# Kernel tuning notes

Hardware: AMD Instinct MI355X
Metric: run time of the kernel (lower is better)

## Reference

```python
import jax, jax.numpy as jnp
import numpy as np

LOG2PI = float(np.log(2.0 * np.pi))

def _sym(M):
    return (M + M.T) * 0.5

def setup_inputs() -> dict:
    key = jax.random.key(0)
    k = jax.random.split(key, 5)
    ntrials, v_dim, T, z_dim = 32, 64, 8192, 16
    v = jax.random.normal(k[0], (ntrials, v_dim, T), jnp.float32)
    # A scaled by 0.2 (instead of raw rand) so the 8192-step recursion stays numerically sane
    A = 0.2 * jax.random.uniform(k[1], (z_dim, z_dim), dtype=jnp.float32)
    B = 0.1 * jnp.eye(z_dim, dtype=jnp.float32)            # as in torch __init__
    W = jax.random.uniform(k[2], (v_dim, z_dim), dtype=jnp.float32)
    mu0 = jax.random.uniform(k[3], (z_dim,), dtype=jnp.float32)
    Sigma0_half = 0.1 * jnp.eye(z_dim, dtype=jnp.float32)  # as in torch __init__
    log_sigma_v = jnp.log(jnp.array([0.5], dtype=jnp.float32))
    return {"v": v, "A": A, "B": B, "W": W, "mu0": mu0,
            "Sigma0_half": Sigma0_half, "log_sigma_v": log_sigma_v}

def reference(v, A, B, W, mu0, Sigma0_half, log_sigma_v):
    # Forward pass used in Preprocessor.fit: kalman_covariance (smoothing=False)
    # + kalman_means (smoothing=False) + LL.  Returns LL per trial [ntrials].
    ntrials, v_dim, T = v.shape
    z_dim = A.shape[0]
    Iz = jnp.eye(z_dim, dtype=v.dtype)
    Iv = jnp.eye(v_dim, dtype=v.dtype)

    var_v = jnp.exp(log_sigma_v[0]) ** 2
    R = var_v * Iv + 1e-6 * Iv                       # property R
    Btri = jnp.tril(B)
    Q = Btri @ Btri.T + 1e-6 * Iz                    # property Q
    S0h = jnp.tril(Sigma0_half)
    Sigma0 = S0h @ S0h.T + 1e-6 * Iz                 # property Sigma0

    def rcho(Lc, X):  # X @ inv(Lc Lc.T), Lc lower cholesky (== chol_inv(..., left=False))
        return jax.scipy.linalg.cho_solve((Lc, True), X.T).T

    # ---- Kalman covariance recursion (data-independent) ----
    L0 = jnp.linalg.cholesky(R + W @ Sigma0 @ W.T)
    K0 = rcho(L0, Sigma0 @ W.T)                      # [z, v]
    Sf0 = _sym(Sigma0 - K0 @ W @ Sigma0)

    def cov_step(Sf, _):
        Sd = _sym(A @ Sf @ A.T + Q)                  # Sigma diffused
        L = jnp.linalg.cholesky(R + W @ Sd @ W.T + 1e-6 * Iv)
        K = rcho(L, Sd @ W.T)
        return _sym(Sd - K @ W @ Sd), (Sd, K)

    _, (Sigmas_diffused, Ks) = jax.lax.scan(cov_step, Sf0, None, length=T - 1)
    # Sigmas_diffused: [T-1, z, z], Ks: [T-1, z, v]

    # ---- Kalman means recursion (vectorized over trials) ----
    vT = jnp.moveaxis(v, -1, 0)                      # [T, ntrials, v_dim]
    muf0 = mu0 + (vT[0] - W @ mu0) @ K0.T            # [ntrials, z]

    def mean_step(muf, inp):
        K, x = inp
        mud = muf @ A.T
        return mud + (x - mud @ W.T) @ K.T, mud

    _, mus_diffused = jax.lax.scan(mean_step, muf0, (Ks, vT[1:]))  # [T-1, n, z]

    # ---- Log likelihood ----
    Lc0 = jnp.linalg.cholesky(W @ Sigma0 @ W.T + R)
    d0 = vT[0] - W @ mu0                             # [n, v]
    s0 = jax.scipy.linalg.solve_triangular(Lc0, d0.T, lower=True)  # [v, n]
    first = (-0.5 * v_dim * LOG2PI
             - jnp.sum(jnp.log(jnp.diag(Lc0)))
             - 0.5 * jnp.sum(s0 ** 2, axis=0))       # [n]

    ms = mus_diffused @ W.T                          # [T-1, n, v]
    covs = jnp.einsum('ij,tjk,lk->til', W, Sigmas_diffused, W) + R + 1e-6 * Iv
    Lt = jnp.linalg.cholesky(covs)                   # [T-1, v, v]
    diff = vT[1:] - ms                               # [T-1, n, v]
    sol = jax.vmap(lambda Lm, dm: jax.scipy.linalg.solve_triangular(Lm, dm.T, lower=True).T)(Lt, diff)
    logdet = jnp.sum(jnp.log(jnp.diagonal(Lt, axis1=-2, axis2=-1)), axis=-1)  # [T-1]
    second = (-0.5 * v_dim * LOG2PI - logdet[:, None]
              - 0.5 * jnp.sum(sol ** 2, axis=-1))    # [T-1, n]
    return first + jnp.sum(second, axis=0)           # [n]
```

## Files before the change

kernel.cpp:

```cpp
#include <hip/hip_runtime.h>
#include <math.h>


#define T_TOT 8192
#define NTR   32
#define VD    64
#define NCHUNK 512
#define CHLEN  16
#define NI     12

#define OFF_FS    8
#define OFF_S     16
#define OFF_P0    272
#define OFF_PSS   528
#define OFF_F     784
#define OFF_M16   1040
#define OFF_KQ    1296
#define OFF_EN0   1552
#define OFF_FQ    2064
#define OFF_VC    2096
#define OFF_QS    (OFF_VC + NCHUNK*512)
#define OFF_Q     (OFF_QS + NCHUNK*32)
#define OFF_XX    (OFF_Q + T_TOT*512)
#define WS_FLOATS (OFF_XX + T_TOT*32 + 64)

__device__ float g_wf[WS_FLOATS];

#define SWZ(x, imm) __int_as_float(__builtin_amdgcn_ds_swizzle(__float_as_int(x), (imm)))

#define MV16(row, vv, out) do { \
  float b0_=SWZ(vv,0x010), b1_=SWZ(vv,0x030), b2_=SWZ(vv,0x050), b3_=SWZ(vv,0x070); \
  float b4_=SWZ(vv,0x090), b5_=SWZ(vv,0x0B0), b6_=SWZ(vv,0x0D0), b7_=SWZ(vv,0x0F0); \
  float b8_=SWZ(vv,0x110), b9_=SWZ(vv,0x130), b10_=SWZ(vv,0x150), b11_=SWZ(vv,0x170); \
  float b12_=SWZ(vv,0x190), b13_=SWZ(vv,0x1B0), b14_=SWZ(vv,0x1D0), b15_=SWZ(vv,0x1F0); \
  float s0_=fmaf((row)[0],b0_,fmaf((row)[1],b1_,fmaf((row)[2],b2_,(row)[3]*b3_))); \
  float s1_=fmaf((row)[4],b4_,fmaf((row)[5],b5_,fmaf((row)[6],b6_,(row)[7]*b7_))); \
  float s2_=fmaf((row)[8],b8_,fmaf((row)[9],b9_,fmaf((row)[10],b10_,(row)[11]*b11_))); \
  float s3_=fmaf((row)[12],b12_,fmaf((row)[13],b13_,fmaf((row)[14],b14_,(row)[15]*b15_))); \
  (out)=(s0_+s1_)+(s2_+s3_); \
} while(0)

#define RED16(x) do { x+=SWZ(x,0x041F); x+=SWZ(x,0x081F); x+=SWZ(x,0x101F); x+=SWZ(x,0x201F); } while(0)

__device__ __forceinline__ void mm_reg(float* C, const float* Aa, const float* Bb, int lane)
{
  const int rowbase = lane & 0x3C;
  const int g = lane & 3;
  #pragma unroll
  for (int j = 0; j < 4; ++j) C[j] = 0.f;
  #pragma unroll
  for (int k = 0; k < 16; ++k) {
    float a = __shfl(Aa[k & 3], rowbase | (k >> 2), 64);
    #pragma unroll
    for (int j = 0; j < 4; ++j) {
      float b = __shfl(Bb[j], 4*k + g, 64);
      C[j] = fmaf(a, b, C[j]);
    }
  }
}

__device__ __forceinline__ void mmbt_reg(float* C, const float* Aa, const float* Bb, int lane)
{
  const int rowbase = lane & 0x3C;
  const int g = lane & 3;
  #pragma unroll
  for (int j = 0; j < 4; ++j) C[j] = 0.f;
  #pragma unroll
  for (int k = 0; k < 16; ++k) {
    float a = __shfl(Aa[k & 3], rowbase | (k >> 2), 64);
    #pragma unroll
    for (int j = 0; j < 4; ++j) {
      float bt = __shfl(Bb[k & 3], 16*g + 4*j + (k >> 2), 64);
      C[j] = fmaf(a, bt, C[j]);
    }
  }
}

__device__ __forceinline__ float gj_reg(float* M, float* R, int lane)
{
  const int i = lane >> 2;
  const int rowbase = lane & 0x3C;
  const int g = lane & 3;
  float ld = 0.f;
  #pragma unroll
  for (int k = 0; k < 16; ++k) {
    float p = __shfl(M[k & 3], 4*k + (k >> 2), 64);
    ld += __logf(fabsf(p));
    float r = 1.f / p;
    float f = __shfl(M[k & 3], rowbase | (k >> 2), 64) * r;
    float t = (i != k) ? f : 0.f;
    #pragma unroll
    for (int j = 0; j < 4; ++j) {
      float mk = __shfl(M[j], 4*k + g, 64);
      float rk = __shfl(R[j], 4*k + g, 64);
      M[j] = fmaf(-t, mk, M[j]);
      R[j] = fmaf(-t, rk, R[j]);
    }
  }
  int e = i & 3;
  float dm = (e & 2) ? ((e & 1) ? M[3] : M[2]) : ((e & 1) ? M[1] : M[0]);
  float d = __shfl(dm, 4*i + (i >> 2), 64);
  float rd = 1.f / d;
  #pragma unroll
  for (int j = 0; j < 4; ++j) R[j] *= rd;
  return ld;
}

__global__ __launch_bounds__(256) void k_front(const float* __restrict__ v,
                                               const float* __restrict__ A,
                                               const float* __restrict__ B,
                                               const float* __restrict__ W,
                                               const float* __restrict__ S0h,
                                               const float* __restrict__ lsv)
{
  const int tid = threadIdx.x;
  float* __restrict__ wf = g_wf;

  if (blockIdx.x != 0) {
    __shared__ float Wl[VD][16];
    for (int e = tid; e < VD*16; e += 256) Wl[e>>4][e&15] = W[e];
    __syncthreads();
    const int bid = blockIdx.x - 1;
    const int n = bid >> 4;
    const int t0 = (bid & 15)*512 + tid*2;
    const float* vp = v + (size_t)n*VD*T_TOT + t0;
    float a0[16], a1[16];
    #pragma unroll
    for (int k = 0; k < 16; ++k) { a0[k] = 0.f; a1[k] = 0.f; }
    float s20 = 0.f, s21 = 0.f;
    #pragma unroll 4
    for (int i2 = 0; i2 < VD; ++i2) {
      float2 x = *(const float2*)&vp[(size_t)i2*T_TOT];
      s20 = fmaf(x.x, x.x, s20); s21 = fmaf(x.y, x.y, s21);
      const float4* wr = (const float4*)&Wl[i2][0];
      float4 w0 = wr[0], w1 = wr[1], w2 = wr[2], w3 = wr[3];
      a0[0]=fmaf(x.x,w0.x,a0[0]);  a1[0]=fmaf(x.y,w0.x,a1[0]);
      a0[1]=fmaf(x.x,w0.y,a0[1]);  a1[1]=fmaf(x.y,w0.y,a1[1]);
      a0[2]=fmaf(x.x,w0.z,a0[2]);  a1[2]=fmaf(x.y,w0.z,a1[2]);
      a0[3]=fmaf(x.x,w0.w,a0[3]);  a1[3]=fmaf(x.y,w0.w,a1[3]);
      a0[4]=fmaf(x.x,w1.x,a0[4]);  a1[4]=fmaf(x.y,w1.x,a1[4]);
      a0[5]=fmaf(x.x,w1.y,a0[5]);  a1[5]=fmaf(x.y,w1.y,a1[5]);
      a0[6]=fmaf(x.x,w1.z,a0[6]);  a1[6]=fmaf(x.y,w1.z,a1[6]);
      a0[7]=fmaf(x.x,w1.w,a0[7]);  a1[7]=fmaf(x.y,w1.w,a1[7]);
      a0[8]=fmaf(x.x,w2.x,a0[8]);  a1[8]=fmaf(x.y,w2.x,a1[8]);
      a0[9]=fmaf(x.x,w2.y,a0[9]);  a1[9]=fmaf(x.y,w2.y,a1[9]);
      a0[10]=fmaf(x.x,w2.z,a0[10]); a1[10]=fmaf(x.y,w2.z,a1[10]);
      a0[11]=fmaf(x.x,w2.w,a0[11]); a1[11]=fmaf(x.y,w2.w,a1[11]);
      a0[12]=fmaf(x.x,w3.x,a0[12]); a1[12]=fmaf(x.y,w3.x,a1[12]);
      a0[13]=fmaf(x.x,w3.y,a0[13]); a1[13]=fmaf(x.y,w3.y,a1[13]);
      a0[14]=fmaf(x.x,w3.z,a0[14]); a1[14]=fmaf(x.y,w3.z,a1[14]);
      a0[15]=fmaf(x.x,w3.w,a0[15]); a1[15]=fmaf(x.y,w3.w,a1[15]);
    }
    float4* q0 = (float4*)(wf + OFF_Q + (size_t)n*131072 + (size_t)t0*16);
    q0[0] = make_float4(a0[0],a0[1],a0[2],a0[3]);
    q0[1] = make_float4(a0[4],a0[5],a0[6],a0[7]);
    q0[2] = make_float4(a0[8],a0[9],a0[10],a0[11]);
    q0[3] = make_float4(a0[12],a0[13],a0[14],a0[15]);
    q0[4] = make_float4(a1[0],a1[1],a1[2],a1[3]);
    q0[5] = make_float4(a1[4],a1[5],a1[6],a1[7]);
    q0[6] = make_float4(a1[8],a1[9],a1[10],a1[11]);
    q0[7] = make_float4(a1[12],a1[13],a1[14],a1[15]);
    wf[OFF_XX + (size_t)n*T_TOT + t0]     = s20;
    wf[OFF_XX + (size_t)n*T_TOT + t0 + 1] = s21;
    return;
  }

  __shared__ float Wl[VD][16];
  __shared__ float Al[16][16], Sm_l[16][16], Qm_l[16][16], S0_l[16][16];
  const int ri = tid >> 4, ci = tid & 15;
  for (int e = tid; e < VD*16; e += 256) Wl[e>>4][e&15] = W[e];
  Al[ri][ci] = A[tid];
  __syncthreads();
  {
    float s = 0.f;
    for (int r = 0; r < VD; ++r) s = fmaf(Wl[r][ri], Wl[r][ci], s);
    Sm_l[ri][ci] = s;
    int m = ri < ci ? ri : ci;
    float q = (ri==ci)?1e-6f:0.f, g0 = (ri==ci)?1e-6f:0.f;
    for (int r = 0; r <= m; ++r) {
      q  = fmaf(B[ri*16+r],   B[ci*16+r],   q);
      g0 = fmaf(S0h[ri*16+r], S0h[ci*16+r], g0);
    }
    Qm_l[ri][ci] = q;
    S0_l[ri][ci] = g0;
  }
  __syncthreads();
  if (tid >= 64) return;

  const int lane = tid;
  const int i = lane >> 2, g = lane & 3;
  float al[4], sm[4], qm[4], s0[4], scl[4], scl0[4], dmask[4];
  {
    float4 t;
    t = *(const float4*)&Al[i][4*g];   al[0]=t.x; al[1]=t.y; al[2]=t.z; al[3]=t.w;
    t = *(const float4*)&Sm_l[i][4*g]; sm[0]=t.x; sm[1]=t.y; sm[2]=t.z; sm[3]=t.w;
    t = *(const float4*)&Qm_l[i][4*g]; qm[0]=t.x; qm[1]=t.y; qm[2]=t.z; qm[3]=t.w;
    t = *(const float4*)&S0_l[i][4*g]; s0[0]=t.x; s0[1]=t.y; s0[2]=t.z; s0[3]=t.w;
  }
  #pragma unroll
  for (int j = 0; j < 4; ++j) dmask[j] = (4*g + j == i) ? 1.f : 0.f;

  float ev = expf(lsv[0]); float var = ev*ev;
  float c0v = var + 1e-6f, cv = var + 2e-6f;
  float invc0 = 1.f/c0v, invc = 1.f/cv;
  float logc = __logf(cv);
  #pragma unroll
  for (int j = 0; j < 4; ++j) { scl0[j] = sm[j]*invc0; scl[j] = sm[j]*invc; }

  float gm[4];
  mm_reg(gm, s0, scl0, lane);
  #pragma unroll
  for (int j = 0; j < 4; ++j) gm[j] += dmask[j];
  float ld0 = gj_reg(gm, s0, lane);
  float ldet_first = 0.5f*(64.f*__logf(c0v) + ld0);
  {
    float4* w4;
    w4 = (float4*)(wf + OFF_P0 + i*16 + 4*g); *w4 = make_float4(s0[0],s0[1],s0[2],s0[3]);
    w4 = (float4*)(wf + OFF_S  + i*16 + 4*g); *w4 = make_float4(sm[0],sm[1],sm[2],sm[3]);
  }

  float p[4];
  #pragma unroll
  for (int j = 0; j < 4; ++j) p[j] = s0[j];

  double dacc = 0.0; float ld_t = 0.f;
  float t1[4], sd[4];
  #pragma unroll 1
  for (int t = 0; t < NI; ++t) {
    mm_reg(t1, al, p, lane);
    mmbt_reg(sd, t1, al, lane);
    #pragma unroll
    for (int j = 0; j < 4; ++j) sd[j] += qm[j];
    mm_reg(gm, sd, scl, lane);
    #pragma unroll
    for (int j = 0; j < 4; ++j) gm[j] += dmask[j];
    float ldG = gj_reg(gm, sd, lane);
    #pragma unroll
    for (int j = 0; j < 4; ++j) p[j] = sd[j];
    ld_t = 0.5f*(64.f*logc + ldG);
    dacc += (double)ld_t;
  }
  double ldet_total = dacc + (double)(T_TOT-1-NI)*(double)ld_t;

  float kq[4], fm_[4], tB[4];
  mm_reg(t1, al, p, lane);
  #pragma unroll
  for (int j = 0; j < 4; ++j) kq[j] = t1[j]*invc;
  mm_reg(tB, kq, sm, lane);
  #pragma unroll
  for (int j = 0; j < 4; ++j) fm_[j] = al[j] - tB[j];
  {
    float4* w4;
    w4 = (float4*)(wf + OFF_PSS + i*16 + 4*g); *w4 = make_float4(p[0],p[1],p[2],p[3]);
    w4 = (float4*)(wf + OFF_F   + i*16 + 4*g); *w4 = make_float4(fm_[0],fm_[1],fm_[2],fm_[3]);
    w4 = (float4*)(wf + OFF_KQ  + i*16 + 4*g); *w4 = make_float4(kq[0],kq[1],kq[2],kq[3]);
  }
  mm_reg(t1, fm_, fm_, lane);
  mm_reg(tB, t1, t1, lane);
  mm_reg(t1, tB, tB, lane);
  mm_reg(tB, t1, t1, lane);
  {
    float4* w4 = (float4*)(wf + OFF_M16 + i*16 + 4*g);
    *w4 = make_float4(tB[0],tB[1],tB[2],tB[3]);
  }
  if (lane == 0) {
    double* d = (double*)wf;
    d[0] = (double)ldet_first;
    d[1] = ldet_total;
    wf[OFF_FS+0] = c0v; wf[OFF_FS+1] = cv; wf[OFF_FS+2] = invc; wf[OFF_FS+3] = invc0;
  }
}

__global__ __launch_bounds__(256) void k_passA(const float* __restrict__ A,
                                               const float* __restrict__ mu0)
{
  const int tid = threadIdx.x; const int j = tid & 15;
  const int n = blockIdx.y*16 + (tid >> 4);
  float* __restrict__ wf = g_wf;

  if (blockIdx.x == NCHUNK) {
    float Ar[16], Sr[16], P0r[16];
    #pragma unroll
    for (int k = 0; k < 16; ++k) {
      Ar[k]  = A[j*16+k];
      Sr[k]  = wf[OFF_S  + j*16 + k];
      P0r[k] = wf[OFF_P0 + j*16 + k];
    }
    const float invc0 = wf[OFF_FS+3];
    float mu0j = mu0[j];
    float q0  = wf[OFF_Q + (size_t)n*131072 + j];
    float xx0 = wf[OFF_XX + (size_t)n*T_TOT];
    float h0; MV16(Sr, mu0j, h0);
    float u0 = q0 - h0;
    float w0; MV16(P0r, u0, w0);
    float loc = fmaf(-2.f*q0, mu0j, fmaf(mu0j, h0, -(u0*w0*invc0)));
    RED16(loc);
    if (j == 0) wf[OFF_FQ + n] = (xx0 + loc)*invc0;
    float muf = fmaf(w0, invc0, mu0j);
    float en; MV16(Ar, muf, en);
    wf[OFF_EN0 + n*16 + j] = en;
    return;
  }

  const int chunk = blockIdx.x;
  float Fr[16], Kr[16];
  #pragma unroll
  for (int k = 0; k < 16; ++k) {
    Fr[k] = wf[OFF_F  + j*16 + k];
    Kr[k] = wf[OFF_KQ + j*16 + k];
  }
  const int t0 = 1 + CHLEN*chunk;
  const float* qp = wf + OFF_Q + (size_t)n*131072 + (size_t)t0*16 + j;
  float mud = 0.f;
  #pragma unroll
  for (int s = 0; s < CHLEN; ++s) {
    float qj = qp[s*16];
    float g; MV16(Kr, qj, g);
    float fm; MV16(Fr, mud, fm);
    mud = fm + g;
  }
  wf[OFF_VC + chunk*512 + n*16 + j] = mud;
}

__global__ __launch_bounds__(256) void k_passC(const float* __restrict__ A)
{
  const int tid = threadIdx.x; const int j = tid & 15;
  const int n = blockIdx.y*16 + (tid >> 4);
  const int chunk = blockIdx.x;
  float* __restrict__ wf = g_wf;
  float Ar[16], Sr[16], Pr[16], Mr[16];
  #pragma unroll
  for (int k = 0; k < 16; ++k) {
    Ar[k] = A[j*16+k];
    Sr[k] = wf[OFF_S   + j*16 + k];
    Pr[k] = wf[OFF_PSS + j*16 + k];
    Mr[k] = wf[OFF_M16 + j*16 + k];
  }
  const float invc = wf[OFF_FS+2];

  float mud;
  if (chunk == 0) {
    mud = wf[OFF_EN0 + n*16 + j];
  } else {
    float v1 = wf[OFF_VC + (chunk-1)*512 + n*16 + j];
    float x2 = (chunk == 1) ? wf[OFF_EN0 + n*16 + j]
                            : wf[OFF_VC + (chunk-2)*512 + n*16 + j];
    float x3 = (chunk == 2) ? wf[OFF_EN0 + n*16 + j]
             : (chunk >= 3) ? wf[OFF_VC + (chunk-3)*512 + n*16 + j] : 0.f;
    float m3; MV16(Mr, x3, m3);
    float y = x2 + m3;
    float m2; MV16(Mr, y, m2);
    mud = v1 + m2;
  }

  const int t0 = 1 + CHLEN*chunk;
  const int ns = (CHLEN < (T_TOT-1) - t0 + 1) ? CHLEN : ((T_TOT-1) - t0 + 1);
  const float* qp  = wf + OFF_Q  + (size_t)n*131072 + (size_t)t0*16 + j;
  const float* xxp = wf + OFF_XX + (size_t)n*T_TOT + t0;
  float qacc = 0.f;
  #pragma unroll 4
  for (int s = 0; s < CHLEN; ++s) {
    float qj = qp[s*16];
    float xxv = xxp[s];
    float h; MV16(Sr, mud, h);
    float u = qj - h;
    float w; MV16(Pr, u, w);
    float loc = fmaf(-2.f*qj, mud, fmaf(mud, h, -(u*w*invc)));
    RED16(loc);
    if (s < ns) qacc = fmaf(xxv + loc, invc, qacc);
    float tmp = fmaf(w, invc, mud);
    MV16(Ar, tmp, mud);
  }
  if (j == 0) wf[OFF_QS + chunk*32 + n] = qacc;
}

__global__ __launch_bounds__(256) void k_final(float* __restrict__ out)
{
  const int tid = threadIdx.x;
  const int slice = tid >> 5, n = tid & 31;
  const float* wf = g_wf;
  __shared__ double red[8][32];
  double acc = 0.0;
  #pragma unroll 8
  for (int k = 0; k < NCHUNK/8; ++k)
    acc += (double)wf[OFF_QS + (slice*(NCHUNK/8) + k)*32 + n];
  red[slice][n] = acc;
  __syncthreads();
  if (tid < 32) {
    const double* dsc = (const double*)wf;
    double a = (double)wf[OFF_FQ + tid];
    #pragma unroll
    for (int s = 0; s < 8; ++s) a += red[s][tid];
    const double LOG2PI = 1.8378770664093453;
    double ll = -32.0*LOG2PI*(double)T_TOT - dsc[0] - dsc[1] - 0.5*a;
    out[tid] = (float)ll;
  }
}

extern "C" void kernel_launch(void* const* d_in, const int* in_sizes, int n_in,
                              void* d_out, int out_size, void* d_ws, size_t ws_size,
                              hipStream_t stream)
{
  (void)in_sizes; (void)n_in; (void)out_size; (void)d_ws; (void)ws_size;
  const float* v   = (const float*)d_in[0];
  const float* A   = (const float*)d_in[1];
  const float* B   = (const float*)d_in[2];
  const float* W   = (const float*)d_in[3];
  const float* mu0 = (const float*)d_in[4];
  const float* S0h = (const float*)d_in[5];
  const float* lsv = (const float*)d_in[6];
  float* out = (float*)d_out;

  k_front<<<1 + NTR*16, 256, 0, stream>>>(v, A, B, W, S0h, lsv);
  k_passA<<<dim3(NCHUNK+1,2), 256, 0, stream>>>(A, mu0);
  k_passC<<<dim3(NCHUNK,2), 256, 0, stream>>>(A);
  k_final<<<1, 256, 0, stream>>>(out);
}
```

Measured before the change: 182.7 us.

## Use DPP/bpermute matrix ops, fewer warmup iterations, and F/K mean update in passC

Replaces the shuffle-based 16x16 register matrix multiply and Gauss-Jordan helpers with DPP quad broadcasts, ds_bpermute and readlane, and accumulates the determinant as a double product instead of summing per-pivot logs. Cuts the covariance warm-up iterations before steady state is assumed from 12 to 8. In passC, the mean update changes from A·(mud + w·invc) to F·mud + K·q, which matches passA. The Mr load also moves into the chunk>0 branch and the chunk loop is fully unrolled. Together these shorten the serial front kernel and the passC inner loop, but fewer warm-up steps risks a less accurate steady-state covariance.

```diff
diff --git a/kernel.cpp b/kernel.cpp
--- a/kernel.cpp
+++ b/kernel.cpp
@@ -7,7 +7,7 @@
 #define VD    64
 #define NCHUNK 512
 #define CHLEN  16
-#define NI     12
+#define NI     8
 
 #define OFF_FS    8
 #define OFF_S     16
@@ -42,68 +42,57 @@
 
 #define RED16(x) do { x+=SWZ(x,0x041F); x+=SWZ(x,0x081F); x+=SWZ(x,0x101F); x+=SWZ(x,0x201F); } while(0)
 
-__device__ __forceinline__ void mm_reg(float* C, const float* Aa, const float* Bb, int lane)
-{
-  const int rowbase = lane & 0x3C;
-  const int g = lane & 3;
-  #pragma unroll
-  for (int j = 0; j < 4; ++j) C[j] = 0.f;
-  #pragma unroll
-  for (int k = 0; k < 16; ++k) {
-    float a = __shfl(Aa[k & 3], rowbase | (k >> 2), 64);
-    #pragma unroll
-    for (int j = 0; j < 4; ++j) {
-      float b = __shfl(Bb[j], 4*k + g, 64);
-      C[j] = fmaf(a, b, C[j]);
-    }
-  }
-}
-
-__device__ __forceinline__ void mmbt_reg(float* C, const float* Aa, const float* Bb, int lane)
-{
-  const int rowbase = lane & 0x3C;
-  const int g = lane & 3;
-  #pragma unroll
-  for (int j = 0; j < 4; ++j) C[j] = 0.f;
-  #pragma unroll
-  for (int k = 0; k < 16; ++k) {
-    float a = __shfl(Aa[k & 3], rowbase | (k >> 2), 64);
-    #pragma unroll
-    for (int j = 0; j < 4; ++j) {
-      float bt = __shfl(Bb[k & 3], 16*g + 4*j + (k >> 2), 64);
-      C[j] = fmaf(a, bt, C[j]);
-    }
-  }
-}
-
-__device__ __forceinline__ float gj_reg(float* M, float* R, int lane)
-{
-  const int i = lane >> 2;
-  const int rowbase = lane & 0x3C;
-  const int g = lane & 3;
-  float ld = 0.f;
-  #pragma unroll
-  for (int k = 0; k < 16; ++k) {
-    float p = __shfl(M[k & 3], 4*k + (k >> 2), 64);
-    ld += __logf(fabsf(p));
-    float r = 1.f / p;
-    float f = __shfl(M[k & 3], rowbase | (k >> 2), 64) * r;
-    float t = (i != k) ? f : 0.f;
-    #pragma unroll
-    for (int j = 0; j < 4; ++j) {
-      float mk = __shfl(M[j], 4*k + g, 64);
-      float rk = __shfl(R[j], 4*k + g, 64);
-      M[j] = fmaf(-t, mk, M[j]);
-      R[j] = fmaf(-t, rk, R[j]);
-    }
-  }
-  int e = i & 3;
-  float dm = (e & 2) ? ((e & 1) ? M[3] : M[2]) : ((e & 1) ? M[1] : M[0]);
-  float d = __shfl(dm, 4*i + (i >> 2), 64);
-  float rd = 1.f / d;
-  #pragma unroll
-  for (int j = 0; j < 4; ++j) R[j] *= rd;
-  return ld;
+#define DPPQ(x, sel) __int_as_float(__builtin_amdgcn_update_dpp( \
+    0, __float_as_int(x), (sel)*0x55, 0xF, 0xF, true))
+#define RDLANE(x, l) __int_as_float(__builtin_amdgcn_readlane(__float_as_int(x), (l)))
+__device__ __forceinline__ float bperm4(int addr, float v) {
+  return __int_as_float(__builtin_amdgcn_ds_bpermute(addr, __float_as_int(v)));
+}
+
+__device__ __forceinline__ void mmF(float* C, const float* Aa, const float* Bb, int bA)
+{
+  C[0]=0.f; C[1]=0.f; C[2]=0.f; C[3]=0.f;
+#define MMK(k) { float a_ = DPPQ(Aa[(k)&3], ((k)>>2)); int ad_ = bA + 16*(k); \
+    C[0]=fmaf(a_, bperm4(ad_, Bb[0]), C[0]); C[1]=fmaf(a_, bperm4(ad_, Bb[1]), C[1]); \
+    C[2]=fmaf(a_, bperm4(ad_, Bb[2]), C[2]); C[3]=fmaf(a_, bperm4(ad_, Bb[3]), C[3]); }
+  MMK(0) MMK(1) MMK(2) MMK(3) MMK(4) MMK(5) MMK(6) MMK(7)
+  MMK(8) MMK(9) MMK(10) MMK(11) MMK(12) MMK(13) MMK(14) MMK(15)
+#undef MMK
+}
+
+__device__ __forceinline__ void mmbtF(float* C, const float* Aa, const float* Bb, int bT)
+{
+  C[0]=0.f; C[1]=0.f; C[2]=0.f; C[3]=0.f;
+#define MBK(k) { float a_ = DPPQ(Aa[(k)&3], ((k)>>2)); \
+    C[0]=fmaf(a_, bperm4(bT +  0 + 4*((k)>>2), Bb[(k)&3]), C[0]); \
+    C[1]=fmaf(a_, bperm4(bT + 16 + 4*((k)>>2), Bb[(k)&3]), C[1]); \
+    C[2]=fmaf(a_, bperm4(bT + 32 + 4*((k)>>2), Bb[(k)&3]), C[2]); \
+    C[3]=fmaf(a_, bperm4(bT + 48 + 4*((k)>>2), Bb[(k)&3]), C[3]); }
+  MBK(0) MBK(1) MBK(2) MBK(3) MBK(4) MBK(5) MBK(6) MBK(7)
+  MBK(8) MBK(9) MBK(10) MBK(11) MBK(12) MBK(13) MBK(14) MBK(15)
+#undef MBK
+}
+
+__device__ __forceinline__ void gjF(float* M, float* R, int bA, int i, double& dp)
+{
+#define GJK(k) { int ad_ = bA + 16*(k); \
+    float mk0_=bperm4(ad_,M[0]), mk1_=bperm4(ad_,M[1]), mk2_=bperm4(ad_,M[2]), mk3_=bperm4(ad_,M[3]); \
+    float rk0_=bperm4(ad_,R[0]), rk1_=bperm4(ad_,R[1]), rk2_=bperm4(ad_,R[2]), rk3_=bperm4(ad_,R[3]); \
+    float p_ = RDLANE(M[(k)&3], 4*(k)+((k)>>2)); \
+    float f_ = DPPQ(M[(k)&3], ((k)>>2)); \
+    float t_ = (i != (k)) ? f_*(1.f/p_) : 0.f; \
+    dp *= (double)p_; \
+    M[0]=fmaf(-t_,mk0_,M[0]); M[1]=fmaf(-t_,mk1_,M[1]); \
+    M[2]=fmaf(-t_,mk2_,M[2]); M[3]=fmaf(-t_,mk3_,M[3]); \
+    R[0]=fmaf(-t_,rk0_,R[0]); R[1]=fmaf(-t_,rk1_,R[1]); \
+    R[2]=fmaf(-t_,rk2_,R[2]); R[3]=fmaf(-t_,rk3_,R[3]); }
+  GJK(0) GJK(1) GJK(2) GJK(3) GJK(4) GJK(5) GJK(6) GJK(7)
+  GJK(8) GJK(9) GJK(10) GJK(11) GJK(12) GJK(13) GJK(14) GJK(15)
+#undef GJK
+  float dm = (i & 2) ? ((i & 1) ? M[3] : M[2]) : ((i & 1) ? M[1] : M[0]);
+  float d = bperm4((4*i + (i>>2))*4, dm);
+  float rd = 1.f/d;
+  R[0]*=rd; R[1]*=rd; R[2]*=rd; R[3]*=rd;
 }
 
 __global__ __launch_bounds__(256) void k_front(const float* __restrict__ v,
@@ -189,6 +178,7 @@
 
   const int lane = tid;
   const int i = lane >> 2, g = lane & 3;
+  const int bA = 4*g, bT = 64*g;
   float al[4], sm[4], qm[4], s0[4], scl[4], scl0[4], dmask[4];
   {
     float4 t;
@@ -208,11 +198,12 @@
   for (int j = 0; j < 4; ++j) { scl0[j] = sm[j]*invc0; scl[j] = sm[j]*invc; }
 
   float gm[4];
-  mm_reg(gm, s0, scl0, lane);
+  mmF(gm, s0, scl0, bA);
   #pragma unroll
   for (int j = 0; j < 4; ++j) gm[j] += dmask[j];
-  float ld0 = gj_reg(gm, s0, lane);
-  float ldet_first = 0.5f*(64.f*__logf(c0v) + ld0);
+  double dp0 = 1.0;
+  gjF(gm, s0, bA, i, dp0);
+  float ldet_first = 0.5f*(64.f*__logf(c0v) + __logf((float)dp0));
   {
     float4* w4;
     w4 = (float4*)(wf + OFF_P0 + i*16 + 4*g); *w4 = make_float4(s0[0],s0[1],s0[2],s0[3]);
@@ -227,26 +218,27 @@
   float t1[4], sd[4];
   #pragma unroll 1
   for (int t = 0; t < NI; ++t) {
-    mm_reg(t1, al, p, lane);
-    mmbt_reg(sd, t1, al, lane);
+    mmF(t1, al, p, bA);
+    mmbtF(sd, t1, al, bT);
     #pragma unroll
     for (int j = 0; j < 4; ++j) sd[j] += qm[j];
-    mm_reg(gm, sd, scl, lane);
+    mmF(gm, sd, scl, bA);
     #pragma unroll
     for (int j = 0; j < 4; ++j) gm[j] += dmask[j];
-    float ldG = gj_reg(gm, sd, lane);
+    double dp = 1.0;
+    gjF(gm, sd, bA, i, dp);
     #pragma unroll
     for (int j = 0; j < 4; ++j) p[j] = sd[j];
-    ld_t = 0.5f*(64.f*logc + ldG);
+    ld_t = 0.5f*(64.f*logc + __logf((float)dp));
     dacc += (double)ld_t;
   }
   double ldet_total = dacc + (double)(T_TOT-1-NI)*(double)ld_t;
 
   float kq[4], fm_[4], tB[4];
-  mm_reg(t1, al, p, lane);
+  mmF(t1, al, p, bA);
   #pragma unroll
   for (int j = 0; j < 4; ++j) kq[j] = t1[j]*invc;
-  mm_reg(tB, kq, sm, lane);
+  mmF(tB, kq, sm, bA);
   #pragma unroll
   for (int j = 0; j < 4; ++j) fm_[j] = al[j] - tB[j];
   {
@@ -255,10 +247,10 @@
     w4 = (float4*)(wf + OFF_F   + i*16 + 4*g); *w4 = make_float4(fm_[0],fm_[1],fm_[2],fm_[3]);
     w4 = (float4*)(wf + OFF_KQ  + i*16 + 4*g); *w4 = make_float4(kq[0],kq[1],kq[2],kq[3]);
   }
-  mm_reg(t1, fm_, fm_, lane);
-  mm_reg(tB, t1, t1, lane);
-  mm_reg(t1, tB, tB, lane);
-  mm_reg(tB, t1, t1, lane);
+  mmF(t1, fm_, fm_, bA);
+  mmF(tB, t1, t1, bA);
+  mmF(t1, tB, tB, bA);
+  mmF(tB, t1, t1, bA);
   {
     float4* w4 = (float4*)(wf + OFF_M16 + i*16 + 4*g);
     *w4 = make_float4(tB[0],tB[1],tB[2],tB[3]);
@@ -322,19 +314,19 @@
   wf[OFF_VC + chunk*512 + n*16 + j] = mud;
 }
 
-__global__ __launch_bounds__(256) void k_passC(const float* __restrict__ A)
+__global__ __launch_bounds__(256) void k_passC()
 {
   const int tid = threadIdx.x; const int j = tid & 15;
   const int n = blockIdx.y*16 + (tid >> 4);
   const int chunk = blockIdx.x;
   float* __restrict__ wf = g_wf;
-  float Ar[16], Sr[16], Pr[16], Mr[16];
+  float Fr[16], Kr[16], Sr[16], Pr[16];
   #pragma unroll
   for (int k = 0; k < 16; ++k) {
-    Ar[k] = A[j*16+k];
+    Fr[k] = wf[OFF_F   + j*16 + k];
+    Kr[k] = wf[OFF_KQ  + j*16 + k];
     Sr[k] = wf[OFF_S   + j*16 + k];
     Pr[k] = wf[OFF_PSS + j*16 + k];
-    Mr[k] = wf[OFF_M16 + j*16 + k];
   }
   const float invc = wf[OFF_FS+2];
 
@@ -342,6 +334,9 @@
   if (chunk == 0) {
     mud = wf[OFF_EN0 + n*16 + j];
   } else {
+    float Mr[16];
+    #pragma unroll
+    for (int k = 0; k < 16; ++k) Mr[k] = wf[OFF_M16 + j*16 + k];
     float v1 = wf[OFF_VC + (chunk-1)*512 + n*16 + j];
     float x2 = (chunk == 1) ? wf[OFF_EN0 + n*16 + j]
                             : wf[OFF_VC + (chunk-2)*512 + n*16 + j];
@@ -358,7 +353,7 @@
   const float* qp  = wf + OFF_Q  + (size_t)n*131072 + (size_t)t0*16 + j;
   const float* xxp = wf + OFF_XX + (size_t)n*T_TOT + t0;
   float qacc = 0.f;
-  #pragma unroll 4
+  #pragma unroll
   for (int s = 0; s < CHLEN; ++s) {
     float qj = qp[s*16];
     float xxv = xxp[s];
@@ -368,8 +363,9 @@
     float loc = fmaf(-2.f*qj, mud, fmaf(mud, h, -(u*w*invc)));
     RED16(loc);
     if (s < ns) qacc = fmaf(xxv + loc, invc, qacc);
-    float tmp = fmaf(w, invc, mud);
-    MV16(Ar, tmp, mud);
+    float gq; MV16(Kr, qj, gq);
+    float fm; MV16(Fr, mud, fm);
+    mud = fm + gq;
   }
   if (j == 0) wf[OFF_QS + chunk*32 + n] = qacc;
 }
@@ -413,6 +409,6 @@
 
   k_front<<<1 + NTR*16, 256, 0, stream>>>(v, A, B, W, S0h, lsv);
   k_passA<<<dim3(NCHUNK+1,2), 256, 0, stream>>>(A, mu0);
-  k_passC<<<dim3(NCHUNK,2), 256, 0, stream>>>(A);
+  k_passC<<<dim3(NCHUNK,2), 256, 0, stream>>>();
   k_final<<<1, 256, 0, stream>>>(out);
 }
```

Result: faster. 165.9 us (-9.2%).
